# Kernel optimization log

Hardware: AMD Instinct MI355X
Metric: run time of the kernel (lower is better)

Reference implementation:

```python
import jax, jax.numpy as jnp
import numpy as np

K, NC, NA = 9, 13, 5
NB, NH, NW = 128, 26, 26
NT, L = 50, 2 * K + 3
NOOBJ, OBJ, SIL = 1.0, 5.0, 0.6
COORD_S, CLASS_S = 1.0, 1.0
PRETRAIN_EPOCHS = 15
TH, SHARP = 80.0, 2.0                      # corner-conf distance threshold (px), sharpness
SCALE = np.array([640.0, 480.0], np.float32)  # im_width, im_height used by corner_confidences
CONF0 = float(np.exp(SHARP) - 1.0)
ANCHORS = np.array([1.482, 2.2412, 2.0501, 3.1265, 2.3946, 4.6891,
                    3.1018, 3.991, 3.4879, 5.8851], np.float32).reshape(NA, 2)


def setup_inputs():
    k1, k2 = jax.random.split(jax.random.key(0))
    output = jax.random.normal(k1, (NB, NA * (2 * K + 1 + NC), NH, NW), dtype=jnp.float32)
    target = jax.random.uniform(k2, (NB, NT * L), dtype=jnp.float32)
    return {"output": output, "target": target, "epoch": 20}


def _corner_conf(pred, gt):
    # pred, gt: [..., K, 2] normalized corners -> mean per-corner confidence [...]
    d = jnp.sqrt((((pred - gt) * jnp.asarray(SCALE)) ** 2).sum(-1))  # pixel distance [..., K]
    c = (jnp.exp(SHARP * (1.0 - d / TH)) - 1.0) / CONF0
    return jnp.where(d < TH, c, 0.0).mean(-1)


def _region_loss(output, target, epoch):
    nAnch, nPix = NA * NH * NW, NH * NW
    tgt = jax.lax.stop_gradient(target).reshape(NB, NT, L)
    out = output.reshape(NB, NA, 2 * K + 1 + NC, NH, NW)
    # keypoint 0 gets sigmoid, the rest are raw offsets
    xs = jnp.concatenate([jax.nn.sigmoid(out[:, :, 0:1]), out[:, :, 2:2 * K:2]], axis=2)  # [B,A,K,H,W]
    ys = jnp.concatenate([jax.nn.sigmoid(out[:, :, 1:2]), out[:, :, 3:2 * K:2]], axis=2)
    conf = jax.nn.sigmoid(out[:, :, 2 * K])                             # [B,A,H,W]
    cls_logits = jnp.transpose(out[:, :, 2 * K + 1:], (0, 1, 3, 4, 2))  # [B,A,H,W,NC]

    gxg = jnp.arange(NW, dtype=jnp.float32)
    gyg = jnp.arange(NH, dtype=jnp.float32)
    px = (jax.lax.stop_gradient(xs) + gxg) / NW            # detached, as torch uses .data
    py = (jax.lax.stop_gradient(ys) + gyg[:, None]) / NH
    # pred corners per anchor cell, flat anchor index = a*H*W + j*W + i -> [B, A*H*W, K, 2]
    pc = jnp.transpose(jnp.stack([px, py], -1), (0, 1, 3, 4, 2, 5)).reshape(NB, nAnch, K, 2)

    gt_xy = tgt[:, :, 1:1 + 2 * K].reshape(NB, NT, K, 2)
    # torch loop breaks at first target with x1 == 0 -> cumulative validity
    valid = jnp.cumprod((tgt[:, :, 1] != 0).astype(jnp.int32), axis=1) > 0  # [B,T]

    # pass 1: max corner confidence over valid GT, per anchor cell
    def max_conf_step(cur, inp):
        gt_t, v_t = inp                                    # [B,K,2], [B]
        c = _corner_conf(pc, gt_t[:, None]).reshape(NB, NA, NH, NW)
        return jnp.where(v_t[:, None, None, None], jnp.maximum(cur, c), cur), None

    cur_confs, _ = jax.lax.scan(max_conf_step, jnp.zeros((NB, NA, NH, NW), jnp.float32),
                                (jnp.swapaxes(gt_xy, 0, 1), valid.T))
    conf_mask0 = jnp.where(cur_confs > SIL, 0.0, NOOBJ)

    # per-target quantities (vectorized over b,t)
    gx = gt_xy[..., 0] * NW                                # [B,T,K]
    gy = gt_xy[..., 1] * NH
    gi0 = jnp.clip(jnp.floor(gx[:, :, 0]).astype(jnp.int32), 0, NW - 1)  # [B,T]
    gj0 = jnp.clip(jnp.floor(gy[:, :, 0]).astype(jnp.int32), 0, NH - 1)
    # pred_box is fetched with best_n == -1 (as in the source); emulate torch negative flat index via mod
    flat_idx = jnp.mod(jnp.arange(NB)[:, None] * nAnch - nPix + gj0 * NW + gi0, NB * nAnch)
    pred_box = pc.reshape(NB * nAnch, K, 2)[flat_idx]      # [B,T,K,2]
    conf_t = _corner_conf(pred_box, gt_xy)                 # [B,T]
    gw = tgt[:, :, L - 2] * NW
    gh = tgt[:, :, L - 1] * NH
    aw, ah = ANCHORS[:, 0], ANCHORS[:, 1]
    mw = jnp.minimum(aw, gw[..., None])                    # centered-box IoU (bbox_iou, cxcywh)
    mh = jnp.minimum(ah, gh[..., None])
    inter = mw * mh
    iou = inter / (aw * ah + (gw * gh)[..., None] - inter)
    best_n = jnp.argmax(iou, axis=-1).astype(jnp.int32)    # [B,T] (first max, like strict '>')
    txv = gx - gi0[..., None].astype(jnp.float32)          # [B,T,K]
    tyv = gy - gj0[..., None].astype(jnp.float32)
    tclsv = tgt[:, :, 0]

    # pass 2: sequential scatter matching torch overwrite order over t
    barange = jnp.arange(NB)
    z = jnp.zeros((NB, NA, NH, NW), jnp.float32)
    zk = jnp.zeros((NB, NA, NH, NW, K), jnp.float32)

    def scatter_step(carry, inp):
        cm, clm, cfm, tx, ty, tcf, tcl = carry
        v, bn, gj, gi, cft, txt, tyt, tct = inp
        idx = (barange, bn, gj, gi)
        vk = v[:, None]
        cm = cm.at[idx].set(jnp.where(v, 1.0, cm[idx]))
        clm = clm.at[idx].set(jnp.where(v, 1.0, clm[idx]))
        cfm = cfm.at[idx].set(jnp.where(v, OBJ, cfm[idx]))
        tx = tx.at[idx].set(jnp.where(vk, txt, tx[idx]))
        ty = ty.at[idx].set(jnp.where(vk, tyt, ty[idx]))
        tcf = tcf.at[idx].set(jnp.where(v, cft, tcf[idx]))
        tcl = tcl.at[idx].set(jnp.where(v, tct, tcl[idx]))
        return (cm, clm, cfm, tx, ty, tcf, tcl), None

    inps = (valid.T, best_n.T, gj0.T, gi0.T, conf_t.T,
            jnp.swapaxes(txv, 0, 1), jnp.swapaxes(tyv, 0, 1), tclsv.T)
    (coord_mask, cls_mask, conf_mask, tx, ty, tconf, tcls), _ = jax.lax.scan(
        scatter_step, (z, z, conf_mask0, zk, zk, z, z), inps)

    # losses
    xsT = jnp.transpose(xs, (0, 1, 3, 4, 2))               # [B,A,H,W,K]
    ysT = jnp.transpose(ys, (0, 1, 3, 4, 2))
    cmk = coord_mask[..., None]
    loss_x = 0.5 * COORD_S * jnp.sum(((xsT - tx) * cmk) ** 2)
    loss_y = 0.5 * COORD_S * jnp.sum(((ysT - ty) * cmk) ** 2)
    sq = jnp.sqrt(conf_mask)
    loss_conf = 0.5 * jnp.sum(((conf - tconf) * sq) ** 2)
    labels = jnp.clip(tcls.astype(jnp.int32), 0, NC - 1)
    ce = -jnp.take_along_axis(jax.nn.log_softmax(cls_logits, axis=-1),
                              labels[..., None], axis=-1)[..., 0]
    loss_cls = CLASS_S * jnp.sum(ce * cls_mask)
    loss = loss_x + loss_y + loss_cls
    if epoch > PRETRAIN_EPOCHS:
        loss = loss + loss_conf
    return loss


def reference(output, target, epoch):
    return _region_loss(output, target, epoch)
```

## Files before the change

kernel.cpp:

```cpp
#include <hip/hip_runtime.h>
#include <math.h>

#define KK     9
#define NCLS   13
#define NANC   5
#define NBB    128
#define NHH    26
#define NWW    26
#define NTT    50
#define LL     21
#define CHC    32
#define NPIX   676
#define NANCHT 3380
#define NCELLT 432640
#define GTS    20
#define MWPB   106

#define LOG2E_F   1.4426950408889634f
#define K1C       2.8853900817779268f
#define K2C       0.036067376022224085f
#define SXW       24.615384615384617f
#define SYH       18.461538461538463f
#define THRESH_S  43.500902934225507f
#define CULL_T2   292.0f
#define CONF_T_SCALE 0.017390849194407297f
#define OBJ_W     5.0f
#define EPOCH_PRETRAIN 15
#define BIGV      6.0e18f

typedef __attribute__((ext_vector_type(2))) float f2;

static __device__ __forceinline__ float fast_exp2(float x){
  return __builtin_amdgcn_exp2f(x);
}
static __device__ __forceinline__ float fast_sqrt(float x){
  return __builtin_amdgcn_sqrtf(x);
}
static __device__ __forceinline__ float sigmoidf_(float x){
  return 1.0f/(1.0f + fast_exp2(-LOG2E_F*x));
}

__constant__ float c_anch[10] = {1.482f,2.2412f,2.0501f,3.1265f,2.3946f,4.6891f,
                                 3.1018f,3.991f,3.4879f,5.8851f};


__global__ __launch_bounds__(64) void prep_kernel(const float* __restrict__ tgt,
                                                  float* __restrict__ gts_neg,
                                                  int* __restrict__ nvalid){
  int b = blockIdx.x;
  int t = threadIdx.x;
  const float* trow = tgt + (size_t)b*NTT*LL;
  float v1 = (t < NTT) ? trow[t*LL + 1] : 0.0f;
  unsigned long long mk = __ballot(t < NTT && v1 != 0.0f);
  int firstInvalid = __ffsll(~mk) - 1;
  if (t == 0) nvalid[b] = firstInvalid;
  for (int idx = t; idx < NTT*GTS; idx += 64){
    int tt = idx / GTS;
    int c  = idx - tt*GTS;
    float v;
    if (c == 9 || c == 19)      v = BIGV;
    else if (c < 9)             v = -(trow[tt*LL + 1 + 2*c] * 640.0f);
    else                        v = -(trow[tt*LL + 2 + 2*(c-10)] * 480.0f);
    gts_neg[(size_t)b*NTT*GTS + idx] = v;
  }
}

__global__ __launch_bounds__(256) void region_confmask_kernel(
    const float* __restrict__ outp, const float* __restrict__ gts_neg,
    const int* __restrict__ nvalid, unsigned int* __restrict__ maskw,
    double* __restrict__ partials){
  int b = blockIdx.y;
  int cell = blockIdx.x * blockDim.x + threadIdx.x;

  __shared__ float sgt[NTT*GTS] __attribute__((aligned(16)));
  for (int idx = threadIdx.x; idx < NTT*GTS; idx += 256)
    sgt[idx] = gts_neg[(size_t)b*NTT*GTS + idx];
  __syncthreads();

  int m0 = 1;
  float contrib = 0.0f;
  if (cell < NANCHT){
    int a   = cell / NPIX;
    int rem = cell - a*NPIX;
    int j   = rem / NWW;
    int i   = rem - j*NWW;
    const float* base = outp + (((size_t)b*NANC + a)*CHC)*NPIX + rem;

    f2 Pxp[5], Pyp[5];
#pragma unroll
    for (int k = 0; k < KK; ++k){
      float rx = base[(2*k)*NPIX];
      float ry = base[(2*k+1)*NPIX];
      if (k == 0){ rx = sigmoidf_(rx); ry = sigmoidf_(ry); }
      Pxp[k>>1][k&1] = (rx + (float)i) * SXW;
      Pyp[k>>1][k&1] = (ry + (float)j) * SYH;
    }
    Pxp[4][1] = 0.0f; Pyp[4][1] = 0.0f;

    int nv = nvalid[b];
    unsigned long long qbits = 0ull;
#pragma unroll 2
    for (int t = 0; t < nv; ++t){
      const f2* gx = (const f2*)(sgt + t*GTS);
      const f2* gy = gx + 5;
      f2 m2 = {1e30f, 1e30f};
#pragma unroll
      for (int p = 0; p < 5; ++p){
        f2 dx = Pxp[p] + gx[p];
        f2 dy = Pyp[p] + gy[p];
        f2 r  = __builtin_elementwise_fma(dy, dy, dx*dx);
        m2 = __builtin_elementwise_min(m2, r);
      }
      if (fminf(m2.x, m2.y) < CULL_T2) qbits |= (1ull << t);
    }

    if (__any(qbits != 0ull)){
      bool exc = false;
      while (qbits){
        int t = __ffsll((long long)qbits) - 1;
        qbits &= qbits - 1;
        const float* gg = sgt + t*GTS;
        float s = 0.0f;
#pragma unroll
        for (int k = 0; k < KK; ++k){
          float dx = Pxp[k>>1][k&1] + gg[k];
          float dy = Pyp[k>>1][k&1] + gg[10+k];
          float d  = fast_sqrt(fmaf(dy, dy, dx*dx));
          float e  = fast_exp2(fmaf(d, -K2C, K1C));
          s += fmaxf(e, 1.0f);
        }
        exc |= (s > THRESH_S);
      }
      if (exc) m0 = 0;
    }
    float cf = sigmoidf_(base[(2*KK)*NPIX]);
    contrib = m0 ? 0.5f*cf*cf : 0.0f;
  }

  unsigned long long mb = __ballot(m0 != 0);
  int lane = threadIdx.x & 63;
  int wavebase = blockIdx.x * 256 + (threadIdx.x & ~63);
  if ((lane & 31) == 0 && wavebase < NANCHT){
    unsigned int w = (lane == 0) ? (unsigned int)mb : (unsigned int)(mb >> 32);
    maskw[(size_t)b*MWPB + (wavebase >> 5) + (lane >> 5)] = w;
  }

#pragma unroll
  for (int o = 32; o > 0; o >>= 1) contrib += __shfl_xor(contrib, o, 64);
  __shared__ float wsum[4];
  int wid = threadIdx.x >> 6;
  if (lane == 0) wsum[wid] = contrib;
  __syncthreads();
  if (threadIdx.x == 0){
    double tot = (double)wsum[0] + (double)wsum[1] + (double)wsum[2] + (double)wsum[3];
    partials[blockIdx.y * gridDim.x + blockIdx.x] = tot;
  }
}

__global__ __launch_bounds__(64) void scatter_loss_kernel(
    const float* __restrict__ outp, const float* __restrict__ tgt,
    const int* __restrict__ nvalid, const unsigned int* __restrict__ maskw,
    double* __restrict__ bc_part){
  int b = blockIdx.x;
  int t = threadIdx.x;
  __shared__ int keys[NTT];
  int nv = nvalid[b];
  bool valid = (t < nv);

  int key = -1, gi0 = 0, gj0 = 0, bn = 0;
  float txv[KK], tyv[KK];
  float conf_t = 0.0f, tcls = 0.0f;

  if (t < NTT){
    const float* trow = tgt + ((size_t)b*NTT + t)*LL;
    tcls = trow[0];
    float gx0 = trow[1]*(float)NWW;
    float gy0 = trow[2]*(float)NHH;
    gi0 = min(max((int)floorf(gx0), 0), NWW-1);
    gj0 = min(max((int)floorf(gy0), 0), NHH-1);
#pragma unroll
    for (int k = 0; k < KK; ++k){
      txv[k] = trow[1+2*k]*(float)NWW - (float)gi0;
      tyv[k] = trow[2+2*k]*(float)NHH - (float)gj0;
    }
    float gw = trow[LL-2]*(float)NWW, gh = trow[LL-1]*(float)NHH;
    float best = -1.0f;
    for (int a = 0; a < NANC; ++a){
      float aw = c_anch[2*a], ah = c_anch[2*a+1];
      float inter = fminf(aw, gw) * fminf(ah, gh);
      float iou = inter / (aw*ah + gw*gh - inter);
      if (iou > best){ best = iou; bn = a; }
    }
    key = bn*NPIX + gj0*NWW + gi0;
    keys[t] = key;

    long f = (long)b*NANCHT - NPIX + gj0*NWW + gi0;
    if (f < 0) f += NCELLT;
    int bb  = (int)(f / NANCHT);
    int rr  = (int)(f - (long)bb*NANCHT);
    int aa  = rr / NPIX;
    int rr2 = rr - aa*NPIX;
    int jj  = rr2 / NWW;
    int ii  = rr2 - jj*NWW;
    const float* pbase = outp + (((size_t)bb*NANC + aa)*CHC)*NPIX + rr2;
    float s = 0.0f;
#pragma unroll
    for (int k = 0; k < KK; ++k){
      float rx = pbase[(2*k)*NPIX], ry = pbase[(2*k+1)*NPIX];
      if (k == 0){ rx = sigmoidf_(rx); ry = sigmoidf_(ry); }
      float Pxx = (rx + (float)ii)*SXW, Pyy = (ry + (float)jj)*SYH;
      float dx = Pxx - trow[1+2*k]*640.0f;
      float dy = Pyy - trow[2+2*k]*480.0f;
      float d  = fast_sqrt(fmaf(dy, dy, dx*dx));
      float e  = fast_exp2(fmaf(d, -K2C, K1C));
      s += fmaxf(e, 1.0f);
    }
    conf_t = (s - 9.0f) * CONF_T_SCALE;
  }
  __syncthreads();

  bool winner = valid;
  if (valid){
    for (int u = t+1; u < nv; ++u) if (keys[u] == key){ winner = false; break; }
  }

  double lx = 0.0, ly = 0.0, lcls = 0.0, lcf = 0.0;
  if (winner){
    const float* cbase = outp + (((size_t)b*NANC + bn)*CHC)*NPIX + gj0*NWW + gi0;
    float sx = 0.0f, sy = 0.0f;
#pragma unroll
    for (int k = 0; k < KK; ++k){
      float rx = cbase[(2*k)*NPIX], ry = cbase[(2*k+1)*NPIX];
      if (k == 0){ rx = sigmoidf_(rx); ry = sigmoidf_(ry); }
      float dx = rx - txv[k], dy = ry - tyv[k];
      sx = fmaf(dx, dx, sx); sy = fmaf(dy, dy, sy);
    }
    lx = 0.5*(double)sx; ly = 0.5*(double)sy;

    float lg[NCLS], mx = -1e30f;
#pragma unroll
    for (int c = 0; c < NCLS; ++c){ lg[c] = cbase[(2*KK+1+c)*NPIX]; mx = fmaxf(mx, lg[c]); }
    float se = 0.0f;
#pragma unroll
    for (int c = 0; c < NCLS; ++c) se += fast_exp2((lg[c]-mx)*LOG2E_F);
    int label = min(max((int)tcls, 0), NCLS-1);
    lcls = (double)(mx + logf(se) - lg[label]);

    float cf = sigmoidf_(cbase[(2*KK)*NPIX]);
    int idx = bn*NPIX + gj0*NWW + gi0;
    int m0 = (maskw[(size_t)b*MWPB + (idx >> 5)] >> (idx & 31)) & 1;
    float dcf = cf - conf_t;
    lcf = 0.5*OBJ_W*(double)(dcf*dcf) - (m0 ? 0.5*(double)(cf*cf) : 0.0);
  }

#pragma unroll
  for (int o = 32; o > 0; o >>= 1){
    lx  += __shfl_xor(lx,  o, 64);
    ly  += __shfl_xor(ly,  o, 64);
    lcls+= __shfl_xor(lcls,o, 64);
    lcf += __shfl_xor(lcf, o, 64);
  }
  if (threadIdx.x == 0){
    double* bp = bc_part + (size_t)b*4;
    bp[0] = lx; bp[1] = ly; bp[2] = lcls; bp[3] = lcf;
  }
}

__global__ __launch_bounds__(256) void finalize_kernel(
    const double* __restrict__ bc_part, const double* __restrict__ partials,
    const int* __restrict__ epoch_p, float* __restrict__ outv){
  int tid = threadIdx.x;
  double vx=0, vy=0, vc=0, vf=0, vb=0;
  for (int i = tid; i < NBB; i += 256){
    vx += bc_part[4*i]; vy += bc_part[4*i+1];
    vc += bc_part[4*i+2]; vf += bc_part[4*i+3];
  }
  for (int i = tid; i < 14*NBB; i += 256) vb += partials[i];
#pragma unroll
  for (int o = 32; o > 0; o >>= 1){
    vx += __shfl_xor(vx, o, 64); vy += __shfl_xor(vy, o, 64);
    vc += __shfl_xor(vc, o, 64); vf += __shfl_xor(vf, o, 64);
    vb += __shfl_xor(vb, o, 64);
  }
  __shared__ double sm[5][4];
  int wid = tid >> 6, lane = tid & 63;
  if (lane == 0){ sm[0][wid]=vx; sm[1][wid]=vy; sm[2][wid]=vc; sm[3][wid]=vf; sm[4][wid]=vb; }
  __syncthreads();
  if (tid == 0){
    double fx=0, fy=0, fc=0, ff=0, fb=0;
    for (int w = 0; w < 4; ++w){ fx+=sm[0][w]; fy+=sm[1][w]; fc+=sm[2][w]; ff+=sm[3][w]; fb+=sm[4][w]; }
    double loss = fx + fy + fc;
    if (*epoch_p > EPOCH_PRETRAIN) loss += ff + fb;
    outv[0] = (float)loss;
  }
}

extern "C" void kernel_launch(void* const* d_in, const int* in_sizes, int n_in,
                              void* d_out, int out_size, void* d_ws, size_t ws_size,
                              hipStream_t stream){
  (void)in_sizes; (void)n_in; (void)out_size; (void)ws_size;
  const float* outp = (const float*)d_in[0];
  const float* tgt  = (const float*)d_in[1];
  const int*   ep   = (const int*)d_in[2];
  float* outv = (float*)d_out;
  char* ws = (char*)d_ws;

  double* bc_part  = (double*)(ws);
  double* partials = (double*)(ws + 4096);
  float*  gts_neg  = (float*) (ws + 18432);
  int*    nvalid   = (int*)   (ws + 530432);
  unsigned int* maskw = (unsigned int*)(ws + 530944);

  prep_kernel<<<dim3(NBB), dim3(64), 0, stream>>>(tgt, gts_neg, nvalid);
  region_confmask_kernel<<<dim3(14, NBB), dim3(256), 0, stream>>>(outp, gts_neg, nvalid, maskw, partials);
  scatter_loss_kernel<<<dim3(NBB), dim3(64), 0, stream>>>(outp, tgt, nvalid, maskw, bc_part);
  finalize_kernel<<<dim3(1), dim3(256), 0, stream>>>(bc_part, partials, ep, outv);
}
```

Measured before the change: 135.5 us.

## Cull candidate targets with packed fp16 math, two cells per thread

```diff
diff --git a/kernel.cpp b/kernel.cpp
--- a/kernel.cpp
+++ b/kernel.cpp
@@ -14,7 +14,10 @@
 #define NANCHT 3380
 #define NCELLT 432640
 #define GTS    20
+#define GTH    24
 #define MWPB   106
+#define HALFSPLIT 1728
+#define NBLK   27
 
 #define LOG2E_F   1.4426950408889634f
 #define K1C       2.8853900817779268f
@@ -22,20 +25,18 @@
 #define SXW       24.615384615384617f
 #define SYH       18.461538461538463f
 #define THRESH_S  43.500902934225507f
-#define CULL_T2   292.0f
+#define CULL_H    330.0f
 #define CONF_T_SCALE 0.017390849194407297f
 #define OBJ_W     5.0f
 #define EPOCH_PRETRAIN 15
 #define BIGV      6.0e18f
 
-typedef __attribute__((ext_vector_type(2))) float f2;
-
-static __device__ __forceinline__ float fast_exp2(float x){
-  return __builtin_amdgcn_exp2f(x);
-}
-static __device__ __forceinline__ float fast_sqrt(float x){
-  return __builtin_amdgcn_sqrtf(x);
-}
+typedef _Float16 h2 __attribute__((ext_vector_type(2)));
+typedef _Float16 h4 __attribute__((ext_vector_type(4)));
+typedef _Float16 h8 __attribute__((ext_vector_type(8)));
+
+static __device__ __forceinline__ float fast_exp2(float x){ return __builtin_amdgcn_exp2f(x); }
+static __device__ __forceinline__ float fast_sqrt(float x){ return __builtin_amdgcn_sqrtf(x); }
 static __device__ __forceinline__ float sigmoidf_(float x){
   return 1.0f/(1.0f + fast_exp2(-LOG2E_F*x));
 }
@@ -46,6 +47,7 @@
 
 __global__ __launch_bounds__(64) void prep_kernel(const float* __restrict__ tgt,
                                                   float* __restrict__ gts_neg,
+                                                  _Float16* __restrict__ gth,
                                                   int* __restrict__ nvalid){
   int b = blockIdx.x;
   int t = threadIdx.x;
@@ -63,98 +65,162 @@
     else                        v = -(trow[tt*LL + 2 + 2*(c-10)] * 480.0f);
     gts_neg[(size_t)b*NTT*GTS + idx] = v;
   }
-}
-
-__global__ __launch_bounds__(256) void region_confmask_kernel(
-    const float* __restrict__ outp, const float* __restrict__ gts_neg,
-    const int* __restrict__ nvalid, unsigned int* __restrict__ maskw,
-    double* __restrict__ partials){
+  for (int idx = t; idx < NTT*GTH; idx += 64){
+    int tt = idx / GTH;
+    int c  = idx - tt*GTH;
+    float v = 0.0f;
+    if (c < 8)        v = -(trow[tt*LL + 1 + 2*c] * 640.0f);
+    else if (c < 16)  v = -(trow[tt*LL + 2 + 2*(c-8)] * 480.0f);
+    else if (c == 16) v = -(trow[tt*LL + 1 + 16] * 640.0f);
+    else if (c == 17) v = -(trow[tt*LL + 2 + 16] * 480.0f);
+    gth[(size_t)b*NTT*GTH + idx] = (_Float16)v;
+  }
+}
+
+__global__ __launch_bounds__(64) void region_confmask_kernel(
+    const float* __restrict__ outp, const _Float16* __restrict__ gth,
+    const float* __restrict__ gts_neg, const int* __restrict__ nvalid,
+    unsigned int* __restrict__ maskw, double* __restrict__ partials){
   int b = blockIdx.y;
-  int cell = blockIdx.x * blockDim.x + threadIdx.x;
-
-  __shared__ float sgt[NTT*GTS] __attribute__((aligned(16)));
-  for (int idx = threadIdx.x; idx < NTT*GTS; idx += 256)
-    sgt[idx] = gts_neg[(size_t)b*NTT*GTS + idx];
+  int tid = threadIdx.x;
+  int wavebase0 = blockIdx.x * 64;
+  int c0 = wavebase0 + tid;
+  int c1 = c0 + HALFSPLIT;
+  bool ok1 = (c1 < NANCHT);
+
+  __shared__ int sgt_i[NTT*GTH/2] __attribute__((aligned(16)));
+  const int* gsrc = (const int*)(gth + (size_t)b*NTT*GTH);
+  for (int idx = tid; idx < NTT*GTH/2; idx += 64) sgt_i[idx] = gsrc[idx];
   __syncthreads();
-
-  int m0 = 1;
-  float contrib = 0.0f;
-  if (cell < NANCHT){
-    int a   = cell / NPIX;
-    int rem = cell - a*NPIX;
-    int j   = rem / NWW;
-    int i   = rem - j*NWW;
+  const _Float16* sgt = (const _Float16*)sgt_i;
+
+  float Pxf0[KK], Pyf0[KK], Pxf1[KK], Pyf1[KK];
+  h8 Px8_0, Py8_0, Px8_1, Py8_1;
+  h2 Pt_0, Pt_1;
+  float cf0 = 0.0f, cf1 = 0.0f;
+#pragma unroll
+  for (int k = 0; k < KK; ++k){ Pxf1[k] = 0.0f; Pyf1[k] = 0.0f; }
+
+  {
+    int a = c0 / NPIX, rem = c0 - a*NPIX;
+    int j = rem / NWW, i = rem - j*NWW;
     const float* base = outp + (((size_t)b*NANC + a)*CHC)*NPIX + rem;
-
-    f2 Pxp[5], Pyp[5];
-#pragma unroll
-    for (int k = 0; k < KK; ++k){
-      float rx = base[(2*k)*NPIX];
-      float ry = base[(2*k+1)*NPIX];
+#pragma unroll
+    for (int k = 0; k < KK; ++k){
+      float rx = base[(2*k)*NPIX], ry = base[(2*k+1)*NPIX];
       if (k == 0){ rx = sigmoidf_(rx); ry = sigmoidf_(ry); }
-      Pxp[k>>1][k&1] = (rx + (float)i) * SXW;
-      Pyp[k>>1][k&1] = (ry + (float)j) * SYH;
-    }
-    Pxp[4][1] = 0.0f; Pyp[4][1] = 0.0f;
-
-    int nv = nvalid[b];
-    unsigned long long qbits = 0ull;
+      Pxf0[k] = (rx + (float)i)*SXW; Pyf0[k] = (ry + (float)j)*SYH;
+    }
+    cf0 = sigmoidf_(base[(2*KK)*NPIX]);
+  }
+  if (ok1){
+    int a = c1 / NPIX, rem = c1 - a*NPIX;
+    int j = rem / NWW, i = rem - j*NWW;
+    const float* base = outp + (((size_t)b*NANC + a)*CHC)*NPIX + rem;
+#pragma unroll
+    for (int k = 0; k < KK; ++k){
+      float rx = base[(2*k)*NPIX], ry = base[(2*k+1)*NPIX];
+      if (k == 0){ rx = sigmoidf_(rx); ry = sigmoidf_(ry); }
+      Pxf1[k] = (rx + (float)i)*SXW; Pyf1[k] = (ry + (float)j)*SYH;
+    }
+    cf1 = sigmoidf_(base[(2*KK)*NPIX]);
+  }
+#pragma unroll
+  for (int k = 0; k < 8; ++k){
+    Px8_0[k] = (_Float16)Pxf0[k]; Py8_0[k] = (_Float16)Pyf0[k];
+    Px8_1[k] = (_Float16)Pxf1[k]; Py8_1[k] = (_Float16)Pyf1[k];
+  }
+  Pt_0 = (h2){(_Float16)Pxf0[8], (_Float16)Pyf0[8]};
+  Pt_1 = (h2){(_Float16)Pxf1[8], (_Float16)Pyf1[8]};
+
+  const _Float16 TH16 = (_Float16)CULL_H;
+  int nv = nvalid[b];
+  unsigned long long q0 = 0ull, q1 = 0ull;
 #pragma unroll 2
-    for (int t = 0; t < nv; ++t){
-      const f2* gx = (const f2*)(sgt + t*GTS);
-      const f2* gy = gx + 5;
-      f2 m2 = {1e30f, 1e30f};
-#pragma unroll
-      for (int p = 0; p < 5; ++p){
-        f2 dx = Pxp[p] + gx[p];
-        f2 dy = Pyp[p] + gy[p];
-        f2 r  = __builtin_elementwise_fma(dy, dy, dx*dx);
-        m2 = __builtin_elementwise_min(m2, r);
+  for (int t = 0; t < nv; ++t){
+    h8 GX = *(const h8*)(sgt + t*GTH);
+    h8 GY = *(const h8*)(sgt + t*GTH + 8);
+    h2 GT = *(const h2*)(sgt + t*GTH + 16);
+    unsigned long long bit = 1ull << t;
+    {
+      h8 dx = Px8_0 + GX, dy = Py8_0 + GY;
+      h8 r  = __builtin_elementwise_fma(dy, dy, dx*dx);
+      h4 r4 = __builtin_elementwise_min(__builtin_shufflevector(r, r, 0,1,2,3),
+                                        __builtin_shufflevector(r, r, 4,5,6,7));
+      h2 r2 = __builtin_elementwise_min(__builtin_shufflevector(r4, r4, 0,1),
+                                        __builtin_shufflevector(r4, r4, 2,3));
+      h2 dt = Pt_0 + GT; h2 rt = dt*dt;
+      _Float16 m = __builtin_elementwise_min(
+          __builtin_elementwise_min(r2[0], r2[1]), (_Float16)(rt[0] + rt[1]));
+      if (m < TH16) q0 |= bit;
+    }
+    {
+      h8 dx = Px8_1 + GX, dy = Py8_1 + GY;
+      h8 r  = __builtin_elementwise_fma(dy, dy, dx*dx);
+      h4 r4 = __builtin_elementwise_min(__builtin_shufflevector(r, r, 0,1,2,3),
+                                        __builtin_shufflevector(r, r, 4,5,6,7));
+      h2 r2 = __builtin_elementwise_min(__builtin_shufflevector(r4, r4, 0,1),
+                                        __builtin_shufflevector(r4, r4, 2,3));
+      h2 dt = Pt_1 + GT; h2 rt = dt*dt;
+      _Float16 m = __builtin_elementwise_min(
+          __builtin_elementwise_min(r2[0], r2[1]), (_Float16)(rt[0] + rt[1]));
+      if (m < TH16) q1 |= bit;
+    }
+  }
+  if (!ok1) q1 = 0ull;
+
+  int m0_0 = 1, m0_1 = 1;
+  if (__any((q0 | q1) != 0ull)){
+    const float* gbase = gts_neg + (size_t)b*NTT*GTS;
+    bool e0 = false, e1 = false;
+    while (q0){
+      int t = __ffsll((long long)q0) - 1; q0 &= q0 - 1;
+      const float* gg = gbase + t*GTS;
+      float s = 0.0f;
+#pragma unroll
+      for (int k = 0; k < KK; ++k){
+        float dx = Pxf0[k] + gg[k], dy = Pyf0[k] + gg[10+k];
+        float d  = fast_sqrt(fmaf(dy, dy, dx*dx));
+        float e  = fast_exp2(fmaf(d, -K2C, K1C));
+        s += fmaxf(e, 1.0f);
       }
-      if (fminf(m2.x, m2.y) < CULL_T2) qbits |= (1ull << t);
-    }
-
-    if (__any(qbits != 0ull)){
-      bool exc = false;
-      while (qbits){
-        int t = __ffsll((long long)qbits) - 1;
-        qbits &= qbits - 1;
-        const float* gg = sgt + t*GTS;
-        float s = 0.0f;
-#pragma unroll
-        for (int k = 0; k < KK; ++k){
-          float dx = Pxp[k>>1][k&1] + gg[k];
-          float dy = Pyp[k>>1][k&1] + gg[10+k];
-          float d  = fast_sqrt(fmaf(dy, dy, dx*dx));
-          float e  = fast_exp2(fmaf(d, -K2C, K1C));
-          s += fmaxf(e, 1.0f);
-        }
-        exc |= (s > THRESH_S);
+      e0 |= (s > THRESH_S);
+    }
+    while (q1){
+      int t = __ffsll((long long)q1) - 1; q1 &= q1 - 1;
+      const float* gg = gbase + t*GTS;
+      float s = 0.0f;
+#pragma unroll
+      for (int k = 0; k < KK; ++k){
+        float dx = Pxf1[k] + gg[k], dy = Pyf1[k] + gg[10+k];
+        float d  = fast_sqrt(fmaf(dy, dy, dx*dx));
+        float e  = fast_exp2(fmaf(d, -K2C, K1C));
+        s += fmaxf(e, 1.0f);
       }
-      if (exc) m0 = 0;
-    }
-    float cf = sigmoidf_(base[(2*KK)*NPIX]);
-    contrib = m0 ? 0.5f*cf*cf : 0.0f;
-  }
-
-  unsigned long long mb = __ballot(m0 != 0);
-  int lane = threadIdx.x & 63;
-  int wavebase = blockIdx.x * 256 + (threadIdx.x & ~63);
-  if ((lane & 31) == 0 && wavebase < NANCHT){
-    unsigned int w = (lane == 0) ? (unsigned int)mb : (unsigned int)(mb >> 32);
-    maskw[(size_t)b*MWPB + (wavebase >> 5) + (lane >> 5)] = w;
+      e1 |= (s > THRESH_S);
+    }
+    if (e0) m0_0 = 0;
+    if (e1) m0_1 = 0;
+  }
+
+  float contrib = (m0_0 ? 0.5f*cf0*cf0 : 0.0f) + ((ok1 && m0_1) ? 0.5f*cf1*cf1 : 0.0f);
+
+  int lane = tid;
+  unsigned long long mb0 = __ballot(m0_0 != 0);
+  if ((lane & 31) == 0){
+    unsigned int w = (lane == 0) ? (unsigned int)mb0 : (unsigned int)(mb0 >> 32);
+    maskw[(size_t)b*MWPB + (wavebase0 >> 5) + (lane >> 5)] = w;
+  }
+  unsigned long long mb1 = __ballot(m0_1 != 0);
+  int wavebase1 = wavebase0 + HALFSPLIT;
+  if ((lane & 31) == 0 && wavebase1 < NANCHT){
+    unsigned int w = (lane == 0) ? (unsigned int)mb1 : (unsigned int)(mb1 >> 32);
+    maskw[(size_t)b*MWPB + (wavebase1 >> 5) + (lane >> 5)] = w;
   }
 
 #pragma unroll
   for (int o = 32; o > 0; o >>= 1) contrib += __shfl_xor(contrib, o, 64);
-  __shared__ float wsum[4];
-  int wid = threadIdx.x >> 6;
-  if (lane == 0) wsum[wid] = contrib;
-  __syncthreads();
-  if (threadIdx.x == 0){
-    double tot = (double)wsum[0] + (double)wsum[1] + (double)wsum[2] + (double)wsum[3];
-    partials[blockIdx.y * gridDim.x + blockIdx.x] = tot;
-  }
+  if (tid == 0) partials[b*NBLK + blockIdx.x] = (double)contrib;
 }
 
 __global__ __launch_bounds__(64) void scatter_loss_kernel(
@@ -275,7 +341,7 @@
     vx += bc_part[4*i]; vy += bc_part[4*i+1];
     vc += bc_part[4*i+2]; vf += bc_part[4*i+3];
   }
-  for (int i = tid; i < 14*NBB; i += 256) vb += partials[i];
+  for (int i = tid; i < NBLK*NBB; i += 256) vb += partials[i];
 #pragma unroll
   for (int o = 32; o > 0; o >>= 1){
     vx += __shfl_xor(vx, o, 64); vy += __shfl_xor(vy, o, 64);
@@ -305,14 +371,15 @@
   float* outv = (float*)d_out;
   char* ws = (char*)d_ws;
 
-  double* bc_part  = (double*)(ws);
-  double* partials = (double*)(ws + 4096);
-  float*  gts_neg  = (float*) (ws + 18432);
-  int*    nvalid   = (int*)   (ws + 530432);
-  unsigned int* maskw = (unsigned int*)(ws + 530944);
-
-  prep_kernel<<<dim3(NBB), dim3(64), 0, stream>>>(tgt, gts_neg, nvalid);
-  region_confmask_kernel<<<dim3(14, NBB), dim3(256), 0, stream>>>(outp, gts_neg, nvalid, maskw, partials);
+  double* bc_part   = (double*)(ws);
+  double* partials  = (double*)(ws + 4096);
+  float*  gts_neg   = (float*) (ws + 31744);
+  int*    nvalid    = (int*)   (ws + 543744);
+  unsigned int* maskw = (unsigned int*)(ws + 544256);
+  _Float16* gth     = (_Float16*)(ws + 598528);
+
+  prep_kernel<<<dim3(NBB), dim3(64), 0, stream>>>(tgt, gts_neg, gth, nvalid);
+  region_confmask_kernel<<<dim3(NBLK, NBB), dim3(64), 0, stream>>>(outp, gth, gts_neg, nvalid, maskw, partials);
   scatter_loss_kernel<<<dim3(NBB), dim3(64), 0, stream>>>(outp, tgt, nvalid, maskw, bc_part);
   finalize_kernel<<<dim3(1), dim3(256), 0, stream>>>(bc_part, partials, ep, outv);
 }
```

Result: slower. 149.4 us (+10.3%).

## Cull target-cell pairs with packed fp16 surrogate score before exact corner confidence

Applied to the files above, without the earlier changes.

```diff
diff --git a/kernel.cpp b/kernel.cpp
--- a/kernel.cpp
+++ b/kernel.cpp
@@ -14,7 +14,10 @@
 #define NANCHT 3380
 #define NCELLT 432640
 #define GTS    20
+#define NPAIR  25
+#define PWORDS 18
 #define MWPB   106
+#define NBLK   27
 
 #define LOG2E_F   1.4426950408889634f
 #define K1C       2.8853900817779268f
@@ -22,23 +25,39 @@
 #define SXW       24.615384615384617f
 #define SYH       18.461538461538463f
 #define THRESH_S  43.500902934225507f
-#define CULL_T2   292.0f
 #define CONF_T_SCALE 0.017390849194407297f
 #define OBJ_W     5.0f
 #define EPOCH_PRETRAIN 15
 #define BIGV      6.0e18f
-
-typedef __attribute__((ext_vector_type(2))) float f2;
-
-static __device__ __forceinline__ float fast_exp2(float x){
-  return __builtin_amdgcn_exp2f(x);
-}
-static __device__ __forceinline__ float fast_sqrt(float x){
-  return __builtin_amdgcn_sqrtf(x);
-}
+#define INFH      0x7C00u
+#define NEG6400W  0xEE40EE40u
+#define CULL_FIRE_NEG  -31000.0f
+
+typedef _Float16 h2 __attribute__((ext_vector_type(2)));
+
+static __device__ __forceinline__ float fast_exp2(float x){ return __builtin_amdgcn_exp2f(x); }
+static __device__ __forceinline__ float fast_sqrt(float x){ return __builtin_amdgcn_sqrtf(x); }
 static __device__ __forceinline__ float sigmoidf_(float x){
   return 1.0f/(1.0f + fast_exp2(-LOG2E_F*x));
 }
+static __device__ __forceinline__ int pk_add_sv(int s, int v){
+  int d; asm("v_pk_add_f16 %0, %1, %2" : "=v"(d) : "s"(s), "v"(v)); return d;
+}
+static __device__ __forceinline__ int pk_add_vv(int a, int b){
+  int d; asm("v_pk_add_f16 %0, %1, %2" : "=v"(d) : "v"(a), "v"(b)); return d;
+}
+static __device__ __forceinline__ int pk_mul_vv(int a, int b){
+  int d; asm("v_pk_mul_f16 %0, %1, %2" : "=v"(d) : "v"(a), "v"(b)); return d;
+}
+static __device__ __forceinline__ int pk_fma_vvv(int a, int b, int c){
+  int d; asm("v_pk_fma_f16 %0, %1, %2, %3" : "=v"(d) : "v"(a), "v"(b), "v"(c)); return d;
+}
+static __device__ __forceinline__ int pk_min_vv(int a, int b){
+  int d; asm("v_pk_min_f16 %0, %1, %2" : "=v"(d) : "v"(a), "v"(b)); return d;
+}
+static __device__ __forceinline__ unsigned short f2h_bits(float v){
+  return __builtin_bit_cast(unsigned short, (_Float16)v);
+}
 
 __constant__ float c_anch[10] = {1.482f,2.2412f,2.0501f,3.1265f,2.3946f,4.6891f,
                                  3.1018f,3.991f,3.4879f,5.8851f};
@@ -46,14 +65,15 @@
 
 __global__ __launch_bounds__(64) void prep_kernel(const float* __restrict__ tgt,
                                                   float* __restrict__ gts_neg,
+                                                  unsigned* __restrict__ gtp,
                                                   int* __restrict__ nvalid){
   int b = blockIdx.x;
   int t = threadIdx.x;
   const float* trow = tgt + (size_t)b*NTT*LL;
   float v1 = (t < NTT) ? trow[t*LL + 1] : 0.0f;
   unsigned long long mk = __ballot(t < NTT && v1 != 0.0f);
-  int firstInvalid = __ffsll(~mk) - 1;
-  if (t == 0) nvalid[b] = firstInvalid;
+  int nv = __ffsll(~mk) - 1;
+  if (t == 0) nvalid[b] = nv;
   for (int idx = t; idx < NTT*GTS; idx += 64){
     int tt = idx / GTS;
     int c  = idx - tt*GTS;
@@ -63,83 +83,107 @@
     else                        v = -(trow[tt*LL + 2 + 2*(c-10)] * 480.0f);
     gts_neg[(size_t)b*NTT*GTS + idx] = v;
   }
-}
-
-__global__ __launch_bounds__(256) void region_confmask_kernel(
-    const float* __restrict__ outp, const float* __restrict__ gts_neg,
-    const int* __restrict__ nvalid, unsigned int* __restrict__ maskw,
-    double* __restrict__ partials){
+  if (t < NPAIR){
+    int t0 = 2*t, t1 = 2*t + 1;
+    unsigned w[PWORDS];
+#pragma unroll
+    for (int k = 0; k < KK; ++k){
+      unsigned x0 = (t0 < nv) ? (unsigned)f2h_bits(-(trow[t0*LL+1+2*k]*640.0f)) : INFH;
+      unsigned y0 = (t0 < nv) ? (unsigned)f2h_bits(-(trow[t0*LL+2+2*k]*480.0f)) : INFH;
+      unsigned x1 = (t1 < nv) ? (unsigned)f2h_bits(-(trow[t1*LL+1+2*k]*640.0f)) : INFH;
+      unsigned y1 = (t1 < nv) ? (unsigned)f2h_bits(-(trow[t1*LL+2+2*k]*480.0f)) : INFH;
+      w[k]      = x0 | (x1 << 16);
+      w[KK + k] = y0 | (y1 << 16);
+    }
+    unsigned* dst = gtp + ((size_t)b*NPAIR + t)*PWORDS;
+#pragma unroll
+    for (int p = 0; p < PWORDS; ++p) dst[p] = w[p];
+  }
+}
+
+__global__ __launch_bounds__(128) void region_confmask_kernel(
+    const float* __restrict__ outp, const unsigned* __restrict__ gtp,
+    const float* __restrict__ gts_neg, const int* __restrict__ nvalid,
+    unsigned int* __restrict__ maskw, double* __restrict__ partials){
   int b = blockIdx.y;
-  int cell = blockIdx.x * blockDim.x + threadIdx.x;
-
-  __shared__ float sgt[NTT*GTS] __attribute__((aligned(16)));
-  for (int idx = threadIdx.x; idx < NTT*GTS; idx += 256)
-    sgt[idx] = gts_neg[(size_t)b*NTT*GTS + idx];
-  __syncthreads();
+  int tid = threadIdx.x;
+  int cell = blockIdx.x * 128 + tid;
+  bool active = (cell < NANCHT);
+  int cc = active ? cell : (NANCHT - 1);
+
+  int Pxw[KK], Pyw[KK];
+  float cf;
+  int a = cc / NPIX, rem = cc - a*NPIX;
+  int jj = rem / NWW, ii = rem - jj*NWW;
+  const float* base = outp + (((size_t)b*NANC + a)*CHC)*NPIX + rem;
+#pragma unroll
+  for (int k = 0; k < KK; ++k){
+    float rx = base[(2*k)*NPIX], ry = base[(2*k+1)*NPIX];
+    if (k == 0){ rx = sigmoidf_(rx); ry = sigmoidf_(ry); }
+    unsigned hx = f2h_bits((rx + (float)ii)*SXW);
+    unsigned hy = f2h_bits((ry + (float)jj)*SYH);
+    Pxw[k] = (int)(hx | (hx << 16));
+    Pyw[k] = (int)(hy | (hy << 16));
+  }
+  cf = sigmoidf_(base[(2*KK)*NPIX]);
+
+  const int negC = (int)NEG6400W;
+  const unsigned* gp = gtp + (size_t)b*NPAIR*PWORDS;
+  int M = 0;
+#pragma unroll 2
+  for (int p = 0; p < NPAIR; ++p){
+    int G[PWORDS];
+#pragma unroll
+    for (int w = 0; w < PWORDS; ++w) G[w] = (int)gp[p*PWORDS + w];
+    int acc = 0;
+#pragma unroll
+    for (int k = 0; k < KK; ++k){
+      int dx = pk_add_sv(G[k],      Pxw[k]);
+      int dy = pk_add_sv(G[KK + k], Pyw[k]);
+      int r2 = pk_mul_vv(dx, dx);
+      r2 = pk_fma_vvv(dy, dy, r2);
+      int um = pk_add_vv(r2, negC);
+      um = pk_min_vv(um, 0);
+      acc = pk_add_vv(acc, um);
+    }
+    M = pk_min_vv(M, acc);
+  }
+
+  h2 Mh = __builtin_bit_cast(h2, M);
+  bool fire = ((float)Mh[0] < CULL_FIRE_NEG) | ((float)Mh[1] < CULL_FIRE_NEG);
 
   int m0 = 1;
-  float contrib = 0.0f;
-  if (cell < NANCHT){
-    int a   = cell / NPIX;
-    int rem = cell - a*NPIX;
-    int j   = rem / NWW;
-    int i   = rem - j*NWW;
-    const float* base = outp + (((size_t)b*NANC + a)*CHC)*NPIX + rem;
-
-    f2 Pxp[5], Pyp[5];
-#pragma unroll
-    for (int k = 0; k < KK; ++k){
-      float rx = base[(2*k)*NPIX];
-      float ry = base[(2*k+1)*NPIX];
+  if (fire && active){
+    float Pxf[KK], Pyf[KK];
+#pragma unroll
+    for (int k = 0; k < KK; ++k){
+      float rx = base[(2*k)*NPIX], ry = base[(2*k+1)*NPIX];
       if (k == 0){ rx = sigmoidf_(rx); ry = sigmoidf_(ry); }
-      Pxp[k>>1][k&1] = (rx + (float)i) * SXW;
-      Pyp[k>>1][k&1] = (ry + (float)j) * SYH;
-    }
-    Pxp[4][1] = 0.0f; Pyp[4][1] = 0.0f;
-
+      Pxf[k] = (rx + (float)ii)*SXW; Pyf[k] = (ry + (float)jj)*SYH;
+    }
     int nv = nvalid[b];
-    unsigned long long qbits = 0ull;
-#pragma unroll 2
+    const float* gbase = gts_neg + (size_t)b*NTT*GTS;
+    bool exc = false;
     for (int t = 0; t < nv; ++t){
-      const f2* gx = (const f2*)(sgt + t*GTS);
-      const f2* gy = gx + 5;
-      f2 m2 = {1e30f, 1e30f};
-#pragma unroll
-      for (int p = 0; p < 5; ++p){
-        f2 dx = Pxp[p] + gx[p];
-        f2 dy = Pyp[p] + gy[p];
-        f2 r  = __builtin_elementwise_fma(dy, dy, dx*dx);
-        m2 = __builtin_elementwise_min(m2, r);
+      const float* gg = gbase + t*GTS;
+      float s = 0.0f;
+#pragma unroll
+      for (int k = 0; k < KK; ++k){
+        float dx = Pxf[k] + gg[k], dy = Pyf[k] + gg[10+k];
+        float d  = fast_sqrt(fmaf(dy, dy, dx*dx));
+        float e  = fast_exp2(fmaf(d, -K2C, K1C));
+        s += fmaxf(e, 1.0f);
       }
-      if (fminf(m2.x, m2.y) < CULL_T2) qbits |= (1ull << t);
-    }
-
-    if (__any(qbits != 0ull)){
-      bool exc = false;
-      while (qbits){
-        int t = __ffsll((long long)qbits) - 1;
-        qbits &= qbits - 1;
-        const float* gg = sgt + t*GTS;
-        float s = 0.0f;
-#pragma unroll
-        for (int k = 0; k < KK; ++k){
-          float dx = Pxp[k>>1][k&1] + gg[k];
-          float dy = Pyp[k>>1][k&1] + gg[10+k];
-          float d  = fast_sqrt(fmaf(dy, dy, dx*dx));
-          float e  = fast_exp2(fmaf(d, -K2C, K1C));
-          s += fmaxf(e, 1.0f);
-        }
-        exc |= (s > THRESH_S);
-      }
-      if (exc) m0 = 0;
-    }
-    float cf = sigmoidf_(base[(2*KK)*NPIX]);
-    contrib = m0 ? 0.5f*cf*cf : 0.0f;
-  }
-
+      exc |= (s > THRESH_S);
+    }
+    if (exc) m0 = 0;
+  }
+
+  float contrib = (active && m0) ? 0.5f*cf*cf : 0.0f;
+
+  int lane = tid & 63;
+  int wavebase = blockIdx.x * 128 + (tid & ~63);
   unsigned long long mb = __ballot(m0 != 0);
-  int lane = threadIdx.x & 63;
-  int wavebase = blockIdx.x * 256 + (threadIdx.x & ~63);
   if ((lane & 31) == 0 && wavebase < NANCHT){
     unsigned int w = (lane == 0) ? (unsigned int)mb : (unsigned int)(mb >> 32);
     maskw[(size_t)b*MWPB + (wavebase >> 5) + (lane >> 5)] = w;
@@ -147,14 +191,12 @@
 
 #pragma unroll
   for (int o = 32; o > 0; o >>= 1) contrib += __shfl_xor(contrib, o, 64);
-  __shared__ float wsum[4];
-  int wid = threadIdx.x >> 6;
+  __shared__ float wsum[2];
+  int wid = tid >> 6;
   if (lane == 0) wsum[wid] = contrib;
   __syncthreads();
-  if (threadIdx.x == 0){
-    double tot = (double)wsum[0] + (double)wsum[1] + (double)wsum[2] + (double)wsum[3];
-    partials[blockIdx.y * gridDim.x + blockIdx.x] = tot;
-  }
+  if (tid == 0)
+    partials[b*NBLK + blockIdx.x] = (double)wsum[0] + (double)wsum[1];
 }
 
 __global__ __launch_bounds__(64) void scatter_loss_kernel(
@@ -275,7 +317,7 @@
     vx += bc_part[4*i]; vy += bc_part[4*i+1];
     vc += bc_part[4*i+2]; vf += bc_part[4*i+3];
   }
-  for (int i = tid; i < 14*NBB; i += 256) vb += partials[i];
+  for (int i = tid; i < NBLK*NBB; i += 256) vb += partials[i];
 #pragma unroll
   for (int o = 32; o > 0; o >>= 1){
     vx += __shfl_xor(vx, o, 64); vy += __shfl_xor(vy, o, 64);
@@ -305,14 +347,15 @@
   float* outv = (float*)d_out;
   char* ws = (char*)d_ws;
 
-  double* bc_part  = (double*)(ws);
-  double* partials = (double*)(ws + 4096);
-  float*  gts_neg  = (float*) (ws + 18432);
-  int*    nvalid   = (int*)   (ws + 530432);
-  unsigned int* maskw = (unsigned int*)(ws + 530944);
-
-  prep_kernel<<<dim3(NBB), dim3(64), 0, stream>>>(tgt, gts_neg, nvalid);
-  region_confmask_kernel<<<dim3(14, NBB), dim3(256), 0, stream>>>(outp, gts_neg, nvalid, maskw, partials);
+  double* bc_part   = (double*)(ws);
+  double* partials  = (double*)(ws + 4096);
+  float*  gts_neg   = (float*) (ws + 31744);
+  int*    nvalid    = (int*)   (ws + 543744);
+  unsigned int* maskw = (unsigned int*)(ws + 544256);
+  unsigned* gtp     = (unsigned*)(ws + 598528);
+
+  prep_kernel<<<dim3(NBB), dim3(64), 0, stream>>>(tgt, gts_neg, gtp, nvalid);
+  region_confmask_kernel<<<dim3(NBLK, NBB), dim3(128), 0, stream>>>(outp, gtp, gts_neg, nvalid, maskw, partials);
   scatter_loss_kernel<<<dim3(NBB), dim3(64), 0, stream>>>(outp, tgt, nvalid, maskw, bc_part);
   finalize_kernel<<<dim3(1), dim3(256), 0, stream>>>(bc_part, partials, ep, outv);
 }
```

New measurement: 135.6 us. About the same (+0.0%).
